# Kernel optimization log

Measured on AMD Instinct MI355X. Metric: run time of the kernel, lower is better.

The kernel has to match this reference:

```python
import jax, jax.numpy as jnp
import numpy as np

B, T, S, D = 4, 1024, 32, 512


def setup_inputs() -> dict:
    key = jax.random.key(0)
    ks = jax.random.split(key, 8)
    w_scale = (2 * D) ** -0.5  # keep linear outputs O(1)
    return {
        "hist_real": jax.random.normal(ks[0], (B, T, S, D), jnp.float32),
        "hist_imag": jax.random.normal(ks[1], (B, T, S, D), jnp.float32),
        "current_real": jax.random.normal(ks[2], (B, T, D), jnp.float32),
        "current_imag": jax.random.normal(ks[3], (B, T, D), jnp.float32),
        "confidence": jax.random.uniform(ks[4], (B, T), jnp.float32),
        "qW": jax.random.normal(ks[5], (2 * D, D), jnp.float32) * w_scale,
        "qb": jnp.zeros((D,), jnp.float32),
        "kW": jax.random.normal(ks[6], (2 * D, D), jnp.float32) * w_scale,
        "kb": jnp.zeros((D,), jnp.float32),
        "vW": jax.random.normal(ks[7], (2 * D, 2 * D), jnp.float32) * w_scale,
        "vb": jnp.zeros((2 * D,), jnp.float32),
    }


def reference(hist_real, hist_imag, current_real, current_imag, confidence,
              qW, qb, kW, kb, vW, vb):
    d = qW.shape[1]
    scale = d ** -0.5
    # Q projection from concatenated real/imag of current: [B,T,2D] -> [B,T,D]
    cur2 = jnp.concatenate([current_real, current_imag], axis=-1)
    Q = cur2 @ qW + qb
    # History features: [B,T,S,2D]
    H = jnp.concatenate([hist_real, hist_imag], axis=-1)
    K = H @ kW + kb          # [B,T,S,D]
    V = H @ vW + vb          # [B,T,S,2D]
    # One query attends over S history slots
    scores = jnp.einsum('btd,btsd->bts', Q, K) * scale
    scores = scores * confidence[..., None]  # confidence.unsqueeze(-1).unsqueeze(-1)
    w = jax.nn.softmax(scores, axis=-1)
    ctx = jnp.einsum('bts,btse->bte', w, V)  # [B,T,2D]
    out_r = current_real + 0.1 * ctx[..., :d]
    out_i = current_imag + 0.1 * ctx[..., d:]
    return jax.lax.complex(out_r, out_i)
```

## Files before the change

### kernel.cpp

```cpp
#include <hip/hip_runtime.h>
#include <hip/hip_bf16.h>

typedef __hip_bfloat16 bf16;
using f32x4  = __attribute__((ext_vector_type(4))) float;
using short8 = __attribute__((ext_vector_type(8))) short;

#define B_ 4
#define T_ 1024
#define S_ 32
#define D_ 512
#define M_ (B_*T_)
#define E_ (2*D_)

__device__ __forceinline__ void gload_lds16(const void* g, void* l) {
  __builtin_amdgcn_global_load_lds(
      (const __attribute__((address_space(1))) unsigned int*)g,
      (__attribute__((address_space(3))) unsigned int*)l, 16, 0, 0);
}

__device__ __forceinline__ float bfbits(unsigned short u) {
  return __uint_as_float(((unsigned)u) << 16);
}

__global__ void cast_bf16_k(const float* __restrict__ in, bf16* __restrict__ out, int n) {
  int i = blockIdx.x * blockDim.x + threadIdx.x;
  if (i < n) out[i] = __float2bfloat16(in[i]);
}

__global__ void concat_cast_k(const float* __restrict__ re, const float* __restrict__ im,
                              bf16* __restrict__ out) {
  int g = blockIdx.x * blockDim.x + threadIdx.x;
  int i = g >> 10, e = g & 1023;
  float v = (e < D_) ? re[(size_t)i * D_ + e] : im[(size_t)i * D_ + (e - D_)];
  out[g] = __float2bfloat16(v);
}

__global__ __launch_bounds__(256)
void transpose_cast_k(const float* __restrict__ in, bf16* __restrict__ out, int R, int C) {
  __shared__ float t[32][33];
  int tx = threadIdx.x & 31, ty = threadIdx.x >> 5;
  int r0 = blockIdx.y * 32, c0 = blockIdx.x * 32;
#pragma unroll
  for (int j = 0; j < 4; ++j)
    t[ty + 8 * j][tx] = in[(size_t)(r0 + ty + 8 * j) * C + c0 + tx];
  __syncthreads();
#pragma unroll
  for (int j = 0; j < 4; ++j)
    out[(size_t)(c0 + ty + 8 * j) * R + r0 + tx] = __float2bfloat16(t[tx][ty + 8 * j]);
}

template<int MODE>
__global__ __launch_bounds__(256)
void gemm_bt(const bf16* __restrict__ A, const bf16* __restrict__ Bm,
             int M, int N, int K,
             const float* __restrict__ bias,
             bf16* __restrict__ outB,
             const float* __restrict__ curR, const float* __restrict__ curI,
             float* __restrict__ outC) {
  __shared__ bf16 sA[128 * 64];
  __shared__ bf16 sB[128 * 64];
  const int tid = threadIdx.x, lane = tid & 63, wid = tid >> 6;
  const int bm = blockIdx.y, bn = blockIdx.x;
  const int wm = wid >> 1, wn = wid & 1;
  const int r16 = lane & 15, h = lane >> 4;

  f32x4 acc[4][4];
#pragma unroll
  for (int m = 0; m < 4; ++m)
#pragma unroll
    for (int n = 0; n < 4; ++n) acc[m][n] = (f32x4){0.f, 0.f, 0.f, 0.f};

  for (int k0 = 0; k0 < K; k0 += 64) {
    __syncthreads();
#pragma unroll
    for (int is = 0; is < 4; ++is) {
      int u = wid * 256 + is * 64 + lane;
      int row = u >> 3, c8 = (u & 7) * 8;
      char* dA = (char*)sA + (wid * 256 + is * 64) * 16;
      char* dB = (char*)sB + (wid * 256 + is * 64) * 16;
      gload_lds16(A  + (size_t)(bm * 128 + row) * K + k0 + c8, dA);
      gload_lds16(Bm + (size_t)(bn * 128 + row) * K + k0 + c8, dB);
    }
    __syncthreads();
#pragma unroll
    for (int kk = 0; kk < 2; ++kk) {
      short8 a[4], b[4];
#pragma unroll
      for (int m = 0; m < 4; ++m)
        a[m] = *(const short8*)(sA + (wm * 64 + m * 16 + r16) * 64 + kk * 32 + h * 8);
#pragma unroll
      for (int n = 0; n < 4; ++n)
        b[n] = *(const short8*)(sB + (wn * 64 + n * 16 + r16) * 64 + kk * 32 + h * 8);
#pragma unroll
      for (int m = 0; m < 4; ++m)
#pragma unroll
        for (int n = 0; n < 4; ++n)
          acc[m][n] = __builtin_amdgcn_mfma_f32_16x16x32_bf16(a[m], b[n], acc[m][n], 0, 0, 0);
    }
  }

#pragma unroll
  for (int m = 0; m < 4; ++m)
#pragma unroll
    for (int n = 0; n < 4; ++n) {
      int col = bn * 128 + wn * 64 + n * 16 + r16;
#pragma unroll
      for (int r = 0; r < 4; ++r) {
        int row = bm * 128 + wm * 64 + m * 16 + h * 4 + r;
        float v = acc[m][n][r];
        if (MODE == 0) {
          outB[(size_t)row * N + col] = __float2bfloat16(v + bias[col]);
        } else if (MODE == 1) {
          outB[(size_t)row * N + col] = __float2bfloat16(v);
        } else if (MODE == 2) {
          float vv = v + bias[col];
          if (col < D_)
            outC[(size_t)row * E_ + 2 * col] = curR[(size_t)row * D_ + col] + 0.1f * vv;
          else
            outC[(size_t)row * E_ + 2 * (col - D_) + 1] =
                curI[(size_t)row * D_ + (col - D_)] + 0.1f * vv;
        } else {
          float vv = v + bias[col];
          outC[(size_t)row * D_ + col] = curR[(size_t)row * D_ + col] + 0.1f * vv;
        }
      }
    }
}

__global__ __launch_bounds__(256)
void qkb_k(const bf16* __restrict__ Qb, const float* __restrict__ kb, float* __restrict__ qkb) {
  int lane = threadIdx.x & 63;
  int row = blockIdx.x * 4 + (threadIdx.x >> 6);
  float p = 0.f;
#pragma unroll
  for (int k = 0; k < 8; ++k) {
    int d = lane + 64 * k;
    p += __bfloat162float(Qb[(size_t)row * D_ + d]) * kb[d];
  }
#pragma unroll
  for (int off = 32; off > 0; off >>= 1) p += __shfl_xor(p, off);
  if (lane == 0) qkb[row] = p;
}

__global__ __launch_bounds__(1024)
void attn_k(const float* __restrict__ histR, const float* __restrict__ histI,
            const bf16* __restrict__ Qp, const float* __restrict__ qkb,
            const float* __restrict__ conf, bf16* __restrict__ Hw) {
  __shared__ float scp[S_][4];
  __shared__ float ctxp[4][E_];
  const int i = blockIdx.x;
  const int tid = threadIdx.x;
  const int u = tid & 255, g = tid >> 8;
  const int lane = tid & 63, wg = (tid >> 6) & 3;
  const int s0 = 8 * g;

  float q[4];
  {
    ushort4 qv = *(const ushort4*)((const unsigned short*)Qp + (size_t)i * E_ + 4 * u);
    q[0] = bfbits(qv.x); q[1] = bfbits(qv.y); q[2] = bfbits(qv.z); q[3] = bfbits(qv.w);
  }

  const float* base = (u < 128)
      ? histR + (size_t)i * S_ * D_ + 4 * u
      : histI + (size_t)i * S_ * D_ + 4 * u - D_;
  float4 H4[8];
#pragma unroll
  for (int si = 0; si < 8; ++si)
    H4[si] = *(const float4*)(base + (size_t)(s0 + si) * D_);

#pragma unroll
  for (int si = 0; si < 8; ++si) {
    float p = q[0] * H4[si].x + q[1] * H4[si].y + q[2] * H4[si].z + q[3] * H4[si].w;
#pragma unroll
    for (int off = 32; off > 0; off >>= 1) p += __shfl_xor(p, off);
    if (lane == 0) scp[s0 + si][wg] = p;
  }
  __syncthreads();

  const float cf = conf[i], add = qkb[i];
  const float scale = 0.044194173824159216f;
  float mx = -1e30f;
#pragma unroll
  for (int s = 0; s < S_; ++s) {
    float v = (scp[s][0] + scp[s][1] + scp[s][2] + scp[s][3] + add) * scale * cf;
    mx = fmaxf(mx, v);
  }
  float l = 0.f;
#pragma unroll
  for (int s = 0; s < S_; ++s) {
    float v = (scp[s][0] + scp[s][1] + scp[s][2] + scp[s][3] + add) * scale * cf;
    l += __expf(v - mx);
  }
  const float inv = 1.f / l;
  float wv[8];
#pragma unroll
  for (int si = 0; si < 8; ++si) {
    int s = s0 + si;
    float v = (scp[s][0] + scp[s][1] + scp[s][2] + scp[s][3] + add) * scale * cf;
    wv[si] = __expf(v - mx);
  }

  f32x4 c = (f32x4){0.f, 0.f, 0.f, 0.f};
#pragma unroll
  for (int si = 0; si < 8; ++si) {
    c[0] += wv[si] * H4[si].x;
    c[1] += wv[si] * H4[si].y;
    c[2] += wv[si] * H4[si].z;
    c[3] += wv[si] * H4[si].w;
  }
  *(f32x4*)&ctxp[g][4 * u] = c;
  __syncthreads();

  float r = (ctxp[0][tid] + ctxp[1][tid] + ctxp[2][tid] + ctxp[3][tid]) * inv;
  Hw[(size_t)i * E_ + tid] = __float2bfloat16(r);
}

extern "C" void kernel_launch(void* const* d_in, const int* in_sizes, int n_in,
                              void* d_out, int out_size, void* d_ws, size_t ws_size,
                              hipStream_t stream) {
  const float* histR = (const float*)d_in[0];
  const float* histI = (const float*)d_in[1];
  const float* curR  = (const float*)d_in[2];
  const float* curI  = (const float*)d_in[3];
  const float* conf  = (const float*)d_in[4];
  const float* qW    = (const float*)d_in[5];
  const float* qb    = (const float*)d_in[6];
  const float* kW    = (const float*)d_in[7];
  const float* kb    = (const float*)d_in[8];
  const float* vW    = (const float*)d_in[9];
  const float* vb    = (const float*)d_in[10];
  float* out = (float*)d_out;

  char* ws = (char*)d_ws;
  bf16*  cur2b = (bf16*)ws;
  bf16*  Hwb   = cur2b;
  bf16*  vWT   = (bf16*)(ws + ( 8u << 20));
  bf16*  Qb    = (bf16*)(ws + (10u << 20));
  bf16*  Qpb   = (bf16*)(ws + (14u << 20));
  bf16*  qWT   = (bf16*)(ws + (22u << 20));
  bf16*  kWb   = (bf16*)(ws + (23u << 20));
  float* qkbv  = (float*)(ws + (24u << 20));

  concat_cast_k<<<(M_ * E_) / 256, 256, 0, stream>>>(curR, curI, cur2b);
  cast_bf16_k<<<(E_ * D_) / 256, 256, 0, stream>>>(kW, kWb, E_ * D_);
  transpose_cast_k<<<dim3(D_ / 32, E_ / 32), 256, 0, stream>>>(qW, qWT, E_, D_);
  transpose_cast_k<<<dim3(E_ / 32, E_ / 32), 256, 0, stream>>>(vW, vWT, E_, E_);

  gemm_bt<0><<<dim3(D_ / 128, M_ / 128), 256, 0, stream>>>(
      cur2b, qWT, M_, D_, E_, qb, Qb, nullptr, nullptr, nullptr);
  qkb_k<<<M_ / 4, 256, 0, stream>>>(Qb, kb, qkbv);
  gemm_bt<1><<<dim3(E_ / 128, M_ / 128), 256, 0, stream>>>(
      Qb, kWb, M_, E_, D_, nullptr, Qpb, nullptr, nullptr, nullptr);
  attn_k<<<M_, 1024, 0, stream>>>(histR, histI, Qpb, qkbv, conf, Hwb);

  if (out_size == M_ * D_) {
    gemm_bt<3><<<dim3(D_ / 128, M_ / 128), 256, 0, stream>>>(
        Hwb, vWT, M_, E_, E_, vb, nullptr, curR, curI, out);
  } else {
    gemm_bt<2><<<dim3(E_ / 128, M_ / 128), 256, 0, stream>>>(
        Hwb, vWT, M_, E_, E_, vb, nullptr, curR, curI, out);
  }
}
```

Baseline: 648.0 us.

## Precompute combined kW·qW weight, shrink GEMM tiles, halve attention block size

Reassociates the query path by forming Wkq = kW·qWᵀ once (a 1024x1024x512 GEMM) so each row's key-space query comes from a single GEMM on cur2 instead of two chained GEMMs. The bias terms are folded into precomputed vectors (u, v2) and the per-row qkb dot now reads cur2. All GEMMs move from 128x128 to 64x64 tiles, giving more blocks on the GPU. The attention kernel runs 512 threads, each loading 8 elements per slot. Risks: the combined GEMM does more FLOPs per row (K=1024, N=1024 instead of two smaller ones), bf16 rounding of Wkq changes numerics, and smaller tiles reduce data reuse.

```diff
diff --git a/kernel.cpp b/kernel.cpp
--- a/kernel.cpp
+++ b/kernel.cpp
@@ -22,11 +22,6 @@
   return __uint_as_float(((unsigned)u) << 16);
 }
 
-__global__ void cast_bf16_k(const float* __restrict__ in, bf16* __restrict__ out, int n) {
-  int i = blockIdx.x * blockDim.x + threadIdx.x;
-  if (i < n) out[i] = __float2bfloat16(in[i]);
-}
-
 __global__ void concat_cast_k(const float* __restrict__ re, const float* __restrict__ im,
                               bf16* __restrict__ out) {
   int g = blockIdx.x * blockDim.x + threadIdx.x;
@@ -35,6 +30,13 @@
   out[g] = __float2bfloat16(v);
 }
 
+__global__ void cast2_k(const float* __restrict__ a, const float* __restrict__ b,
+                        bf16* __restrict__ ab, bf16* __restrict__ bb, int n) {
+  int i = blockIdx.x * blockDim.x + threadIdx.x;
+  if (i < n) ab[i] = __float2bfloat16(a[i]);
+  else if (i < 2 * n) bb[i - n] = __float2bfloat16(b[i - n]);
+}
+
 __global__ __launch_bounds__(256)
 void transpose_cast_k(const float* __restrict__ in, bf16* __restrict__ out, int R, int C) {
   __shared__ float t[32][33];
@@ -49,64 +51,106 @@
     out[(size_t)(c0 + ty + 8 * j) * R + r0 + tx] = __float2bfloat16(t[tx][ty + 8 * j]);
 }
 
+__global__ __launch_bounds__(256)
+void uvec_k(const float* __restrict__ qW, const float* __restrict__ kb,
+            const float* __restrict__ kW, const float* __restrict__ qb,
+            float* __restrict__ u, float* __restrict__ v2) {
+  int lane = threadIdx.x & 63, w = threadIdx.x >> 6;
+  int which = blockIdx.x >= 256;
+  int e = ((blockIdx.x & 255) << 2) + w;
+  const float* src = which ? kW : qW;
+  const float* vec = which ? qb : kb;
+  float p = 0.f;
+#pragma unroll
+  for (int k = 0; k < 8; ++k) {
+    int d = lane + 64 * k;
+    p += src[(size_t)e * D_ + d] * vec[d];
+  }
+#pragma unroll
+  for (int off = 32; off > 0; off >>= 1) p += __shfl_xor(p, off);
+  if (lane == 0) (which ? v2 : u)[e] = p;
+}
+
+__global__ __launch_bounds__(256)
+void qkb_k(const bf16* __restrict__ cur2, const float* __restrict__ u,
+           const float* __restrict__ qb, const float* __restrict__ kb,
+           float* __restrict__ qkb) {
+  int lane = threadIdx.x & 63;
+  int row = blockIdx.x * 4 + (threadIdx.x >> 6);
+  float p = 0.f;
+#pragma unroll
+  for (int k = 0; k < 16; ++k) {
+    int d = lane + 64 * k;
+    p += __bfloat162float(cur2[(size_t)row * E_ + d]) * u[d];
+  }
+#pragma unroll
+  for (int k = 0; k < 8; ++k) {
+    int d = lane + 64 * k;
+    p += qb[d] * kb[d];
+  }
+#pragma unroll
+  for (int off = 32; off > 0; off >>= 1) p += __shfl_xor(p, off);
+  if (lane == 0) qkb[row] = p;
+}
+
 template<int MODE>
 __global__ __launch_bounds__(256)
-void gemm_bt(const bf16* __restrict__ A, const bf16* __restrict__ Bm,
-             int M, int N, int K,
-             const float* __restrict__ bias,
-             bf16* __restrict__ outB,
-             const float* __restrict__ curR, const float* __restrict__ curI,
-             float* __restrict__ outC) {
-  __shared__ bf16 sA[128 * 64];
-  __shared__ bf16 sB[128 * 64];
+void gemm64(const bf16* __restrict__ A, const bf16* __restrict__ Bm,
+            int M, int N, int K,
+            const float* __restrict__ bias,
+            bf16* __restrict__ outB,
+            const float* __restrict__ curR, const float* __restrict__ curI,
+            float* __restrict__ outC) {
+  __shared__ bf16 sA[64 * 64];
+  __shared__ bf16 sB[64 * 64];
   const int tid = threadIdx.x, lane = tid & 63, wid = tid >> 6;
   const int bm = blockIdx.y, bn = blockIdx.x;
   const int wm = wid >> 1, wn = wid & 1;
   const int r16 = lane & 15, h = lane >> 4;
 
-  f32x4 acc[4][4];
-#pragma unroll
-  for (int m = 0; m < 4; ++m)
-#pragma unroll
-    for (int n = 0; n < 4; ++n) acc[m][n] = (f32x4){0.f, 0.f, 0.f, 0.f};
+  f32x4 acc[2][2];
+#pragma unroll
+  for (int m = 0; m < 2; ++m)
+#pragma unroll
+    for (int n = 0; n < 2; ++n) acc[m][n] = (f32x4){0.f, 0.f, 0.f, 0.f};
 
   for (int k0 = 0; k0 < K; k0 += 64) {
     __syncthreads();
 #pragma unroll
-    for (int is = 0; is < 4; ++is) {
-      int u = wid * 256 + is * 64 + lane;
-      int row = u >> 3, c8 = (u & 7) * 8;
-      char* dA = (char*)sA + (wid * 256 + is * 64) * 16;
-      char* dB = (char*)sB + (wid * 256 + is * 64) * 16;
-      gload_lds16(A  + (size_t)(bm * 128 + row) * K + k0 + c8, dA);
-      gload_lds16(Bm + (size_t)(bn * 128 + row) * K + k0 + c8, dB);
+    for (int is = 0; is < 2; ++is) {
+      int unit = is * 256 + tid;
+      int row = unit >> 3, c8 = (unit & 7) * 8;
+      char* dA = (char*)sA + (is * 256 + wid * 64) * 16;
+      char* dB = (char*)sB + (is * 256 + wid * 64) * 16;
+      gload_lds16(A  + (size_t)(bm * 64 + row) * K + k0 + c8, dA);
+      gload_lds16(Bm + (size_t)(bn * 64 + row) * K + k0 + c8, dB);
     }
     __syncthreads();
 #pragma unroll
     for (int kk = 0; kk < 2; ++kk) {
-      short8 a[4], b[4];
-#pragma unroll
-      for (int m = 0; m < 4; ++m)
-        a[m] = *(const short8*)(sA + (wm * 64 + m * 16 + r16) * 64 + kk * 32 + h * 8);
-#pragma unroll
-      for (int n = 0; n < 4; ++n)
-        b[n] = *(const short8*)(sB + (wn * 64 + n * 16 + r16) * 64 + kk * 32 + h * 8);
-#pragma unroll
-      for (int m = 0; m < 4; ++m)
-#pragma unroll
-        for (int n = 0; n < 4; ++n)
+      short8 a[2], b[2];
+#pragma unroll
+      for (int m = 0; m < 2; ++m)
+        a[m] = *(const short8*)(sA + (wm * 32 + m * 16 + r16) * 64 + kk * 32 + h * 8);
+#pragma unroll
+      for (int n = 0; n < 2; ++n)
+        b[n] = *(const short8*)(sB + (wn * 32 + n * 16 + r16) * 64 + kk * 32 + h * 8);
+#pragma unroll
+      for (int m = 0; m < 2; ++m)
+#pragma unroll
+        for (int n = 0; n < 2; ++n)
           acc[m][n] = __builtin_amdgcn_mfma_f32_16x16x32_bf16(a[m], b[n], acc[m][n], 0, 0, 0);
     }
   }
 
 #pragma unroll
-  for (int m = 0; m < 4; ++m)
-#pragma unroll
-    for (int n = 0; n < 4; ++n) {
-      int col = bn * 128 + wn * 64 + n * 16 + r16;
+  for (int m = 0; m < 2; ++m)
+#pragma unroll
+    for (int n = 0; n < 2; ++n) {
+      int col = bn * 64 + wn * 32 + n * 16 + r16;
 #pragma unroll
       for (int r = 0; r < 4; ++r) {
-        int row = bm * 128 + wm * 64 + m * 16 + h * 4 + r;
+        int row = bm * 64 + wm * 32 + m * 16 + h * 4 + r;
         float v = acc[m][n][r];
         if (MODE == 0) {
           outB[(size_t)row * N + col] = __float2bfloat16(v + bias[col]);
@@ -127,53 +171,43 @@
     }
 }
 
-__global__ __launch_bounds__(256)
-void qkb_k(const bf16* __restrict__ Qb, const float* __restrict__ kb, float* __restrict__ qkb) {
-  int lane = threadIdx.x & 63;
-  int row = blockIdx.x * 4 + (threadIdx.x >> 6);
-  float p = 0.f;
-#pragma unroll
-  for (int k = 0; k < 8; ++k) {
-    int d = lane + 64 * k;
-    p += __bfloat162float(Qb[(size_t)row * D_ + d]) * kb[d];
-  }
-#pragma unroll
-  for (int off = 32; off > 0; off >>= 1) p += __shfl_xor(p, off);
-  if (lane == 0) qkb[row] = p;
-}
-
-__global__ __launch_bounds__(1024)
+__global__ __launch_bounds__(512)
 void attn_k(const float* __restrict__ histR, const float* __restrict__ histI,
             const bf16* __restrict__ Qp, const float* __restrict__ qkb,
             const float* __restrict__ conf, bf16* __restrict__ Hw) {
-  __shared__ float scp[S_][4];
+  __shared__ float scp[S_][2];
   __shared__ float ctxp[4][E_];
   const int i = blockIdx.x;
   const int tid = threadIdx.x;
-  const int u = tid & 255, g = tid >> 8;
-  const int lane = tid & 63, wg = (tid >> 6) & 3;
+  const int u = tid & 127, g = tid >> 7;
+  const int lane = tid & 63, half = u >> 6;
   const int s0 = 8 * g;
 
-  float q[4];
+  const float* base = (u < 64)
+      ? histR + (size_t)i * S_ * D_ + 8 * u
+      : histI + (size_t)i * S_ * D_ + 8 * u - D_;
+  float4 hp[16];
+#pragma unroll
+  for (int si = 0; si < 8; ++si) {
+    hp[2 * si]     = *(const float4*)(base + (size_t)(s0 + si) * D_);
+    hp[2 * si + 1] = *(const float4*)(base + (size_t)(s0 + si) * D_ + 4);
+  }
+
+  float q[8];
   {
-    ushort4 qv = *(const ushort4*)((const unsigned short*)Qp + (size_t)i * E_ + 4 * u);
-    q[0] = bfbits(qv.x); q[1] = bfbits(qv.y); q[2] = bfbits(qv.z); q[3] = bfbits(qv.w);
-  }
-
-  const float* base = (u < 128)
-      ? histR + (size_t)i * S_ * D_ + 4 * u
-      : histI + (size_t)i * S_ * D_ + 4 * u - D_;
-  float4 H4[8];
-#pragma unroll
-  for (int si = 0; si < 8; ++si)
-    H4[si] = *(const float4*)(base + (size_t)(s0 + si) * D_);
+    ushort4 qa = *(const ushort4*)((const unsigned short*)Qp + (size_t)i * E_ + 8 * u);
+    ushort4 qc = *(const ushort4*)((const unsigned short*)Qp + (size_t)i * E_ + 8 * u + 4);
+    q[0] = bfbits(qa.x); q[1] = bfbits(qa.y); q[2] = bfbits(qa.z); q[3] = bfbits(qa.w);
+    q[4] = bfbits(qc.x); q[5] = bfbits(qc.y); q[6] = bfbits(qc.z); q[7] = bfbits(qc.w);
+  }
 
 #pragma unroll
   for (int si = 0; si < 8; ++si) {
-    float p = q[0] * H4[si].x + q[1] * H4[si].y + q[2] * H4[si].z + q[3] * H4[si].w;
+    float p = q[0] * hp[2*si].x + q[1] * hp[2*si].y + q[2] * hp[2*si].z + q[3] * hp[2*si].w
+            + q[4] * hp[2*si+1].x + q[5] * hp[2*si+1].y + q[6] * hp[2*si+1].z + q[7] * hp[2*si+1].w;
 #pragma unroll
     for (int off = 32; off > 0; off >>= 1) p += __shfl_xor(p, off);
-    if (lane == 0) scp[s0 + si][wg] = p;
+    if (lane == 0) scp[s0 + si][half] = p;
   }
   __syncthreads();
 
@@ -181,38 +215,36 @@
   const float scale = 0.044194173824159216f;
   float mx = -1e30f;
 #pragma unroll
-  for (int s = 0; s < S_; ++s) {
-    float v = (scp[s][0] + scp[s][1] + scp[s][2] + scp[s][3] + add) * scale * cf;
-    mx = fmaxf(mx, v);
-  }
+  for (int s = 0; s < S_; ++s)
+    mx = fmaxf(mx, (scp[s][0] + scp[s][1] + add) * scale * cf);
   float l = 0.f;
 #pragma unroll
-  for (int s = 0; s < S_; ++s) {
-    float v = (scp[s][0] + scp[s][1] + scp[s][2] + scp[s][3] + add) * scale * cf;
-    l += __expf(v - mx);
-  }
+  for (int s = 0; s < S_; ++s)
+    l += __expf((scp[s][0] + scp[s][1] + add) * scale * cf - mx);
   const float inv = 1.f / l;
   float wv[8];
 #pragma unroll
+  for (int si = 0; si < 8; ++si)
+    wv[si] = __expf((scp[s0 + si][0] + scp[s0 + si][1] + add) * scale * cf - mx);
+
+  f32x4 c0 = (f32x4){0.f,0.f,0.f,0.f}, c1 = (f32x4){0.f,0.f,0.f,0.f};
+#pragma unroll
   for (int si = 0; si < 8; ++si) {
-    int s = s0 + si;
-    float v = (scp[s][0] + scp[s][1] + scp[s][2] + scp[s][3] + add) * scale * cf;
-    wv[si] = __expf(v - mx);
-  }
-
-  f32x4 c = (f32x4){0.f, 0.f, 0.f, 0.f};
-#pragma unroll
-  for (int si = 0; si < 8; ++si) {
-    c[0] += wv[si] * H4[si].x;
-    c[1] += wv[si] * H4[si].y;
-    c[2] += wv[si] * H4[si].z;
-    c[3] += wv[si] * H4[si].w;
-  }
-  *(f32x4*)&ctxp[g][4 * u] = c;
+    c0[0] += wv[si] * hp[2*si].x;  c0[1] += wv[si] * hp[2*si].y;
+    c0[2] += wv[si] * hp[2*si].z;  c0[3] += wv[si] * hp[2*si].w;
+    c1[0] += wv[si] * hp[2*si+1].x; c1[1] += wv[si] * hp[2*si+1].y;
+    c1[2] += wv[si] * hp[2*si+1].z; c1[3] += wv[si] * hp[2*si+1].w;
+  }
+  *(f32x4*)&ctxp[g][8 * u] = c0;
+  *(f32x4*)&ctxp[g][8 * u + 4] = c1;
   __syncthreads();
 
-  float r = (ctxp[0][tid] + ctxp[1][tid] + ctxp[2][tid] + ctxp[3][tid]) * inv;
-  Hw[(size_t)i * E_ + tid] = __float2bfloat16(r);
+  int e = 2 * tid;
+  float r0 = (ctxp[0][e] + ctxp[1][e] + ctxp[2][e] + ctxp[3][e]) * inv;
+  float r1 = (ctxp[0][e+1] + ctxp[1][e+1] + ctxp[2][e+1] + ctxp[3][e+1]) * inv;
+  bf16* dst = Hw + (size_t)i * E_ + e;
+  dst[0] = __float2bfloat16(r0);
+  dst[1] = __float2bfloat16(r1);
 }
 
 extern "C" void kernel_launch(void* const* d_in, const int* in_sizes, int n_in,
@@ -233,31 +265,33 @@
 
   char* ws = (char*)d_ws;
   bf16*  cur2b = (bf16*)ws;
-  bf16*  Hwb   = cur2b;
-  bf16*  vWT   = (bf16*)(ws + ( 8u << 20));
-  bf16*  Qb    = (bf16*)(ws + (10u << 20));
-  bf16*  Qpb   = (bf16*)(ws + (14u << 20));
-  bf16*  qWT   = (bf16*)(ws + (22u << 20));
-  bf16*  kWb   = (bf16*)(ws + (23u << 20));
-  float* qkbv  = (float*)(ws + (24u << 20));
+  bf16*  Qpb   = (bf16*)(ws + ( 8u << 20));
+  bf16*  Hwb   = (bf16*)(ws + (16u << 20));
+  bf16*  Wkq   = (bf16*)(ws + (24u << 20));
+  bf16*  vWT   = (bf16*)(ws + (26u << 20));
+  bf16*  qWb   = (bf16*)(ws + (28u << 20));
+  bf16*  kWb   = (bf16*)(ws + (29u << 20));
+  float* uvec  = (float*)(ws + (30u << 20));
+  float* v2vec = (float*)(ws + (30u << 20) + 16384);
+  float* qkbv  = (float*)(ws + (30u << 20) + 32768);
 
   concat_cast_k<<<(M_ * E_) / 256, 256, 0, stream>>>(curR, curI, cur2b);
-  cast_bf16_k<<<(E_ * D_) / 256, 256, 0, stream>>>(kW, kWb, E_ * D_);
-  transpose_cast_k<<<dim3(D_ / 32, E_ / 32), 256, 0, stream>>>(qW, qWT, E_, D_);
+  cast2_k<<<(2 * E_ * D_) / 256, 256, 0, stream>>>(qW, kW, qWb, kWb, E_ * D_);
   transpose_cast_k<<<dim3(E_ / 32, E_ / 32), 256, 0, stream>>>(vW, vWT, E_, E_);
-
-  gemm_bt<0><<<dim3(D_ / 128, M_ / 128), 256, 0, stream>>>(
-      cur2b, qWT, M_, D_, E_, qb, Qb, nullptr, nullptr, nullptr);
-  qkb_k<<<M_ / 4, 256, 0, stream>>>(Qb, kb, qkbv);
-  gemm_bt<1><<<dim3(E_ / 128, M_ / 128), 256, 0, stream>>>(
-      Qb, kWb, M_, E_, D_, nullptr, Qpb, nullptr, nullptr, nullptr);
-  attn_k<<<M_, 1024, 0, stream>>>(histR, histI, Qpb, qkbv, conf, Hwb);
+  uvec_k<<<512, 256, 0, stream>>>(qW, kb, kW, qb, uvec, v2vec);
+
+  gemm64<1><<<dim3(E_ / 64, E_ / 64), 256, 0, stream>>>(
+      kWb, qWb, E_, E_, D_, nullptr, Wkq, nullptr, nullptr, nullptr);
+  qkb_k<<<M_ / 4, 256, 0, stream>>>(cur2b, uvec, qb, kb, qkbv);
+  gemm64<0><<<dim3(E_ / 64, M_ / 64), 256, 0, stream>>>(
+      cur2b, Wkq, M_, E_, E_, v2vec, Qpb, nullptr, nullptr, nullptr);
+  attn_k<<<M_, 512, 0, stream>>>(histR, histI, Qpb, qkbv, conf, Hwb);
 
   if (out_size == M_ * D_) {
-    gemm_bt<3><<<dim3(D_ / 128, M_ / 128), 256, 0, stream>>>(
+    gemm64<3><<<dim3(D_ / 64, M_ / 64), 256, 0, stream>>>(
         Hwb, vWT, M_, E_, E_, vb, nullptr, curR, curI, out);
   } else {
-    gemm_bt<2><<<dim3(E_ / 128, M_ / 128), 256, 0, stream>>>(
+    gemm64<2><<<dim3(E_ / 64, M_ / 64), 256, 0, stream>>>(
         Hwb, vWT, M_, E_, E_, vb, nullptr, curR, curI, out);
   }
 }
```

New measurement: 601.6 us. -7.2%, faster.
